# Kernel optimization log

Measured on AMD Instinct MI355X. Metric: run time of the kernel, lower is better.

The kernel has to match this reference:

```python
import jax, jax.numpy as jnp
import numpy as np

B, N, DIM = 1, 1024, 512
H, DH = 8, 64
TOPK_RATIO = 0.1
SCALE = DH ** -0.5
PH = 32  # phase MLP hidden = hidden_dim//2 = 64//2
INIT_SCALE = 0.02


def cayley(Mre, Mim):
    # CayleyLinear: unitary weight W = (I - A)^{-1} (I + A), A skew-Hermitian
    M = (Mre + 1j * Mim).astype(jnp.complex64) * INIT_SCALE
    A = M - M.conj().T
    I = jnp.eye(M.shape[0], dtype=M.dtype)
    return jnp.linalg.solve(I - A, I + A)


def phase_fn(mag, pw1, pb1, pw2, pb2):
    # PhaseModulation: MLP(|alpha|) + 0.1*|alpha| residual
    h = jax.nn.silu(mag[..., None] @ pw1 + pb1)  # (...,PH)
    out = (h @ pw2 + pb2)[..., 0]
    return out + mag * 0.1


def setup_inputs() -> dict:
    key = jax.random.key(0)
    ks = jax.random.split(key, 12)
    d = {
        'x_real': jax.random.normal(ks[0], (B, N, DIM), dtype=jnp.float32),
        'x_imag': jax.random.normal(ks[1], (B, N, DIM), dtype=jnp.float32),
    }
    for i, n in enumerate(['Wq', 'Wk', 'Wv', 'Wo']):
        d[n + '_re'] = jax.random.normal(ks[2 + 2 * i], (DIM, DIM), dtype=jnp.float32)
        d[n + '_im'] = jax.random.normal(ks[3 + 2 * i], (DIM, DIM), dtype=jnp.float32)
    d['pw1'] = jax.random.normal(ks[10], (1, PH), dtype=jnp.float32) * 0.1
    d['pb1'] = jnp.zeros((PH,), dtype=jnp.float32)
    d['pw2'] = jax.random.normal(ks[11], (PH, 1), dtype=jnp.float32) * 0.1
    d['pb2'] = jnp.zeros((1,), dtype=jnp.float32)
    return d


def reference(x_real, x_imag, Wq_re, Wq_im, Wk_re, Wk_im, Wv_re, Wv_im,
              Wo_re, Wo_im, pw1, pb1, pw2, pb2):
    x = (x_real + 1j * x_imag).astype(jnp.complex64)  # (B,N,D)
    Q = x @ cayley(Wq_re, Wq_im)
    K = x @ cayley(Wk_re, Wk_im)
    V = x @ cayley(Wv_re, Wv_im)
    # (B,N,D) -> (B,H,N,DH)
    Q = Q.reshape(B, N, H, DH).transpose(0, 2, 1, 3)
    K = K.reshape(B, N, H, DH).transpose(0, 2, 1, 3)
    V = V.reshape(B, N, H, DH).transpose(0, 2, 1, 3)
    # complex inner products: conj(Q) . K
    alpha = jnp.einsum('bhnd,bhsd->bhns', Q.conj(), K) * SCALE  # (B,H,N,N) complex
    mag = jnp.abs(alpha)
    phase = phase_fn(jax.lax.stop_gradient(mag), pw1, pb1, pw2, pb2)
    beta = alpha * jnp.exp(1j * phase.astype(jnp.complex64))
    # Born-rule normalization: p = |beta|^2 / sum |beta|^2
    b2 = beta.real ** 2 + beta.imag ** 2
    probs = b2 / b2.sum(axis=-1, keepdims=True)  # (B,H,N,N) real
    # top-k interference routing
    k = max(1, int(TOPK_RATIO * N))
    tp, ti = jax.lax.top_k(probs, k)  # (B,H,N,k)
    tpn = tp / (tp.sum(axis=-1, keepdims=True) + 1e-8)
    w = jax.nn.softmax(tpn * k, axis=-1)  # complex_softmax on real input
    # gather V rows per (b,h): (N,DH)[(N,k)] -> (N,k,DH), no NxN expand
    gather = jax.vmap(jax.vmap(lambda v, i: v[i]))
    V_topk = gather(V, ti)  # (B,H,N,k,DH) complex
    out = (w[..., None] * V_topk).sum(axis=3)  # (B,H,N,DH)
    out = out.transpose(0, 2, 1, 3).reshape(B, N, DIM)
    out = out @ cayley(Wo_re, Wo_im)
    return out  # complex64 (B,N,DIM)
```

## Files before the change

kernel.cpp:

```cpp
#include <hip/hip_runtime.h>
#include <math.h>


#define PLANE   262144
#define CMAT    524288
#define PPLANE  524288
#define CPROJ   1048576
#define KTOP    102

#define R_FLOATS 12582912
#define POOL_FLOATS (4*CMAT + 8192 + R_FLOATS)
__device__ __attribute__((aligned(256))) float g_pool[POOL_FLOATS];

__launch_bounds__(256)
__global__ void cgemm_kernel(
    const float* __restrict__ Are, const float* __restrict__ Aim, int sA,
    const float* __restrict__ Bre, const float* __restrict__ Bim, int sB,
    const float* __restrict__ Dre, const float* __restrict__ Dim, int sD,
    const float* __restrict__ Ere2, float* __restrict__ Ewr, int sE,
    float* __restrict__ Cre, float* __restrict__ Cim, int sC,
    int M, int N, int Kd, float dcoef, int mode, int out_floats)
{
    __shared__ float As_re[2][32][34], As_im[2][32][34];
    __shared__ float Bs_re[2][32][68], Bs_im[2][32][68];
    const int b = blockIdx.z;
    Are += (size_t)b * sA; Aim += (size_t)b * sA;
    Bre += (size_t)b * sB; Bim += (size_t)b * sB;
    Dre += (size_t)b * sD; Dim += (size_t)b * sD;
    const float* Ere = Ere2 + (size_t)b * sE;
    const float* Eim = Ere + PLANE;
    float* Uwr = Ewr ? (Ewr + (size_t)b * sE) : (float*)0;
    Cre += (size_t)b * sC; Cim += (size_t)b * sC;
    const int bnd = mode == 5 ? (out_floats - b * sC) : 0;
    const int tid = threadIdx.x;
    const int bm = blockIdx.y * 32, bn = blockIdx.x * 64;
    const int tm = (tid >> 4) << 1;
    const int tn = (tid & 15) << 2;
    const int lmA = tid >> 3;
    const int lkA = (tid & 7) << 2;
    const int lkB = tid >> 4;
    const int lnB = (tid & 15) << 2;
    float cr[2][4] = {{0.f}}, ci[2][4] = {{0.f}};
    const float* pAre = Are + (size_t)(bm + lmA) * Kd + lkA;
    const float* pAim = Aim + (size_t)(bm + lmA) * Kd + lkA;
    const float* pBre = Bre + (size_t)lkB * N + bn + lnB;
    const float* pBim = Bim + (size_t)lkB * N + bn + lnB;
    float4 ar  = *(const float4*)(pAre);
    float4 ai  = *(const float4*)(pAim);
    float4 br0 = *(const float4*)(pBre);
    float4 bi0 = *(const float4*)(pBim);
    float4 br1 = *(const float4*)(pBre + (size_t)16 * N);
    float4 bi1 = *(const float4*)(pBim + (size_t)16 * N);
    for (int k0 = 0; k0 < Kd; k0 += 32) {
        const int buf = (k0 >> 5) & 1;
        As_re[buf][lkA+0][lmA] = ar.x; As_re[buf][lkA+1][lmA] = ar.y;
        As_re[buf][lkA+2][lmA] = ar.z; As_re[buf][lkA+3][lmA] = ar.w;
        As_im[buf][lkA+0][lmA] = ai.x; As_im[buf][lkA+1][lmA] = ai.y;
        As_im[buf][lkA+2][lmA] = ai.z; As_im[buf][lkA+3][lmA] = ai.w;
        *(float4*)&Bs_re[buf][lkB][lnB] = br0;
        *(float4*)&Bs_im[buf][lkB][lnB] = bi0;
        *(float4*)&Bs_re[buf][lkB+16][lnB] = br1;
        *(float4*)&Bs_im[buf][lkB+16][lnB] = bi1;
        __syncthreads();
        const int kn = k0 + 32;
        if (kn < Kd) {
            ar  = *(const float4*)(pAre + kn);
            ai  = *(const float4*)(pAim + kn);
            br0 = *(const float4*)(pBre + (size_t)kn * N);
            bi0 = *(const float4*)(pBim + (size_t)kn * N);
            br1 = *(const float4*)(pBre + (size_t)(kn + 16) * N);
            bi1 = *(const float4*)(pBim + (size_t)(kn + 16) * N);
        }
        #pragma unroll
        for (int k = 0; k < 32; ++k) {
            const float2 xr = *(const float2*)&As_re[buf][k][tm];
            const float2 xi = *(const float2*)&As_im[buf][k][tm];
            const float4 yr = *(const float4*)&Bs_re[buf][k][tn];
            const float4 yi = *(const float4*)&Bs_im[buf][k][tn];
            const float axr[2] = {xr.x, xr.y};
            const float axi[2] = {xi.x, xi.y};
            const float byr[4] = {yr.x, yr.y, yr.z, yr.w};
            const float byi[4] = {yi.x, yi.y, yi.z, yi.w};
            #pragma unroll
            for (int i = 0; i < 2; ++i) {
                #pragma unroll
                for (int j = 0; j < 4; ++j) {
                    cr[i][j] += axr[i]*byr[j] - axi[i]*byi[j];
                    ci[i][j] += axr[i]*byi[j] + axi[i]*byr[j];
                }
            }
        }
    }
    #pragma unroll
    for (int i = 0; i < 2; ++i) {
        const int row = bm + tm + i;
        const size_t idx = (size_t)row * N + bn + tn;
        float vr[4] = {cr[i][0], cr[i][1], cr[i][2], cr[i][3]};
        float vi[4] = {ci[i][0], ci[i][1], ci[i][2], ci[i][3]};
        if (mode == 1) {
            const float4 dr4 = *(const float4*)(Dre + idx);
            const float4 di4 = *(const float4*)(Dim + idx);
            const float dr[4] = {dr4.x, dr4.y, dr4.z, dr4.w};
            const float di[4] = {di4.x, di4.y, di4.z, di4.w};
            #pragma unroll
            for (int j = 0; j < 4; ++j) { vr[j] = dcoef*dr[j] - vr[j]; vi[j] = dcoef*di[j] - vi[j]; }
        } else if (mode == 2) {
            const float4 dr4 = *(const float4*)(Dre + idx);
            const float4 di4 = *(const float4*)(Dim + idx);
            const float dr[4] = {dr4.x, dr4.y, dr4.z, dr4.w};
            const float di[4] = {di4.x, di4.y, di4.z, di4.w};
            float ur[4], ui[4];
            #pragma unroll
            for (int j = 0; j < 4; ++j) { ur[j] = 5.5f*dr[j] + 0.5f*vr[j]; ui[j] = 5.5f*di[j] + 0.5f*vi[j]; }
            *(float4*)(Uwr + idx) = make_float4(ur[0], ur[1], ur[2], ur[3]);
            *(float4*)(Uwr + PLANE + idx) = make_float4(ui[0], ui[1], ui[2], ui[3]);
        } else if (mode == 3) {
            const float inv61 = 1.0f/61.5f;
            const float4 sr4 = *(const float4*)(Dre + idx);
            const float4 si4 = *(const float4*)(Dim + idx);
            const float4 s2r = *(const float4*)(Ere + idx);
            const float4 s2i = *(const float4*)(Eim + idx);
            const float sr[4] = {sr4.x, sr4.y, sr4.z, sr4.w};
            const float si[4] = {si4.x, si4.y, si4.z, si4.w};
            const float tr[4] = {s2r.x, s2r.y, s2r.z, s2r.w};
            const float ti[4] = {s2i.x, s2i.y, s2i.z, s2i.w};
            #pragma unroll
            for (int j = 0; j < 4; ++j) {
                const float diag = (row == bn + tn + j) ? 60.5f : 0.0f;
                vr[j] = (diag + 48.f*sr[j] + 23.f*tr[j] + vr[j]) * inv61;
                vi[j] = (       48.f*si[j] + 23.f*ti[j] + vi[j]) * inv61;
            }
        } else if (mode == 4) {
            const float4 dr4 = *(const float4*)(Dre + idx);
            const float4 di4 = *(const float4*)(Dim + idx);
            const float dr[4] = {dr4.x, dr4.y, dr4.z, dr4.w};
            const float di[4] = {di4.x, di4.y, di4.z, di4.w};
            #pragma unroll
            for (int j = 0; j < 4; ++j) {
                const float diag = (row == bn + tn + j) ? 1.0f : 0.0f;
                vr[j] = 2.f*dr[j] + 2.f*vr[j] - diag;
                vi[j] = 2.f*di[j] + 2.f*vi[j];
            }
        }
        if (mode == 5) {
            #pragma unroll
            for (int j = 0; j < 4; ++j) {
                const size_t ire = idx + j;
                const size_t iim = (size_t)PPLANE + idx + j;
                if (ire < (size_t)bnd) Cre[ire] = vr[j];
                if (iim < (size_t)bnd) Cre[iim] = vi[j];
            }
        } else {
            *(float4*)(Cre + idx) = make_float4(vr[0], vr[1], vr[2], vr[3]);
            *(float4*)(Cim + idx) = make_float4(vi[0], vi[1], vi[2], vi[3]);
        }
    }
}

__launch_bounds__(256)
__global__ void build_A_kernel(const float* __restrict__ W0re, const float* __restrict__ W0im,
                               const float* __restrict__ W1re, const float* __restrict__ W1im,
                               const float* __restrict__ W2re, const float* __restrict__ W2im,
                               const float* __restrict__ W3re, const float* __restrict__ W3im,
                               int aoff)
{
    float* Aout = g_pool + aoff;
    const int w = blockIdx.y;
    const float* Mre; const float* Mim;
    if      (w == 0) { Mre = W0re; Mim = W0im; }
    else if (w == 1) { Mre = W1re; Mim = W1im; }
    else if (w == 2) { Mre = W2re; Mim = W2im; }
    else             { Mre = W3re; Mim = W3im; }
    const int idx = blockIdx.x * 256 + threadIdx.x;
    const int i = idx >> 9, j = idx & 511;
    float* Are = Aout + (size_t)w * CMAT;
    float* Aim = Are + PLANE;
    Are[idx] = 0.02f * (Mre[i*512 + j] - Mre[j*512 + i]);
    Aim[idx] = 0.02f * (Mim[i*512 + j] + Mim[j*512 + i]);
}

__launch_bounds__(256)
__global__ void zero_kernel(float* __restrict__ p, int n)
{
    const int i = blockIdx.x * 256 + threadIdx.x;
    if (i < n) p[i] = 0.f;
}

__launch_bounds__(256)
__global__ void scores_kernel(const float* __restrict__ Qre, const float* __restrict__ Qim,
                              const float* __restrict__ Kre, const float* __restrict__ Kim,
                              float* __restrict__ B2, float* __restrict__ RS)
{
    __shared__ float Qs_re[16][68], Qs_im[16][68], Ks_re[16][68], Ks_im[16][68];
    __shared__ float rs[64];
    const int h = blockIdx.z;
    const int bm = blockIdx.y * 64, bn = blockIdx.x * 64;
    const int tid = threadIdx.x;
    const int tm = (tid >> 4) << 2, tn = (tid & 15) << 2;
    const int lm = tid >> 2, lk = (tid & 3) << 2;
    float dr[4][4] = {{0.f}}, di[4][4] = {{0.f}};
    for (int k0 = 0; k0 < 64; k0 += 16) {
        const float4 qr = *(const float4*)(Qre + (size_t)(bm+lm)*512 + h*64 + k0 + lk);
        const float4 qi = *(const float4*)(Qim + (size_t)(bm+lm)*512 + h*64 + k0 + lk);
        const float4 kr = *(const float4*)(Kre + (size_t)(bn+lm)*512 + h*64 + k0 + lk);
        const float4 ki = *(const float4*)(Kim + (size_t)(bn+lm)*512 + h*64 + k0 + lk);
        __syncthreads();
        Qs_re[lk+0][lm]=qr.x; Qs_re[lk+1][lm]=qr.y; Qs_re[lk+2][lm]=qr.z; Qs_re[lk+3][lm]=qr.w;
        Qs_im[lk+0][lm]=qi.x; Qs_im[lk+1][lm]=qi.y; Qs_im[lk+2][lm]=qi.z; Qs_im[lk+3][lm]=qi.w;
        Ks_re[lk+0][lm]=kr.x; Ks_re[lk+1][lm]=kr.y; Ks_re[lk+2][lm]=kr.z; Ks_re[lk+3][lm]=kr.w;
        Ks_im[lk+0][lm]=ki.x; Ks_im[lk+1][lm]=ki.y; Ks_im[lk+2][lm]=ki.z; Ks_im[lk+3][lm]=ki.w;
        __syncthreads();
        #pragma unroll
        for (int k = 0; k < 16; ++k) {
            const float4 xr = *(const float4*)&Qs_re[k][tm];
            const float4 xi = *(const float4*)&Qs_im[k][tm];
            const float4 yr = *(const float4*)&Ks_re[k][tn];
            const float4 yi = *(const float4*)&Ks_im[k][tn];
            const float axr[4] = {xr.x, xr.y, xr.z, xr.w};
            const float axi[4] = {xi.x, xi.y, xi.z, xi.w};
            const float byr[4] = {yr.x, yr.y, yr.z, yr.w};
            const float byi[4] = {yi.x, yi.y, yi.z, yi.w};
            #pragma unroll
            for (int i = 0; i < 4; ++i) {
                #pragma unroll
                for (int j = 0; j < 4; ++j) {
                    dr[i][j] += axr[i]*byr[j] + axi[i]*byi[j];
                    di[i][j] += axr[i]*byi[j] - axi[i]*byr[j];
                }
            }
        }
    }
    if (tid < 64) rs[tid] = 0.f;
    __syncthreads();
    float rpart[4] = {0.f, 0.f, 0.f, 0.f};
    #pragma unroll
    for (int i = 0; i < 4; ++i) {
        #pragma unroll
        for (int j = 0; j < 4; ++j) {
            const float b2v = (dr[i][j]*dr[i][j] + di[i][j]*di[i][j]) * 0.015625f;
            B2[(size_t)h*1048576 + (size_t)(bm+tm+i)*1024 + (bn+tn+j)] = b2v;
            rpart[i] += b2v;
        }
    }
    #pragma unroll
    for (int i = 0; i < 4; ++i) atomicAdd(&rs[tm+i], rpart[i]);
    __syncthreads();
    if (tid < 64) atomicAdd(&RS[h*1024 + bm + tid], rs[tid]);
}

__launch_bounds__(256)
__global__ void select_kernel(const float* __restrict__ B2, const float* __restrict__ RS,
                              const float* __restrict__ Vre, const float* __restrict__ Vim,
                              float* __restrict__ AOre, float* __restrict__ AOim)
{
    __shared__ float sv[1024];
    __shared__ unsigned int hist[256];
    __shared__ int ssum[256];
    __shared__ unsigned int sc[4];
    __shared__ float sel_v[104];
    __shared__ int sel_i[104];
    __shared__ float sel_w[104];
    __shared__ float rbuf[256];
    const int bid = blockIdx.x;
    const int h = bid >> 10, n = bid & 1023;
    const int tid = threadIdx.x;
    const float* row = B2 + (size_t)h * 1048576 + (size_t)n * 1024;
    #pragma unroll
    for (int e = 0; e < 4; ++e) sv[tid + 256*e] = row[tid + 256*e];
    if (tid == 0) sc[2] = 0u;
    __syncthreads();

    unsigned prefix = 0u, pmask = 0u;
    int krem = KTOP;
    for (int pass = 0; pass < 4; ++pass) {
        const int shift = 24 - 8 * pass;
        hist[tid] = 0u;
        __syncthreads();
        #pragma unroll
        for (int e = 0; e < 4; ++e) {
            const unsigned u = __float_as_uint(sv[tid + 256*e]);
            if ((u & pmask) == prefix) atomicAdd(&hist[(u >> shift) & 255u], 1u);
        }
        __syncthreads();
        ssum[tid] = (int)hist[tid];
        __syncthreads();
        for (int off = 1; off < 256; off <<= 1) {
            const int add = (tid + off < 256) ? ssum[tid + off] : 0;
            __syncthreads();
            ssum[tid] += add;
            __syncthreads();
        }
        const int above = (tid < 255) ? ssum[tid + 1] : 0;
        if (ssum[tid] >= krem && above < krem) {
            sc[0] = (unsigned)tid;
            sc[1] = (unsigned)(krem - above);
        }
        __syncthreads();
        prefix |= sc[0] << shift;
        pmask |= 0xFFu << shift;
        krem = (int)sc[1];
        __syncthreads();
    }
    const unsigned T = prefix;
    const int m = krem;

    #pragma unroll
    for (int e = 0; e < 4; ++e) {
        const int i = tid + 256*e;
        const float v = sv[i];
        const unsigned u = __float_as_uint(v);
        bool sel = (u > T);
        if (!sel && u == T) {
            int rank = 0;
            for (int j = 0; j < i; ++j) rank += (__float_as_uint(sv[j]) == T) ? 1 : 0;
            sel = (rank < m);
        }
        if (sel) {
            const unsigned p = atomicAdd(&sc[2], 1u);
            if (p < 104u) { sel_v[p] = v; sel_i[p] = i; }
        }
    }
    __syncthreads();

    rbuf[tid] = (tid < KTOP) ? sel_v[tid] : 0.f;
    __syncthreads();
    for (int st = 128; st > 0; st >>= 1) { if (tid < st) rbuf[tid] += rbuf[tid + st]; __syncthreads(); }
    const float sumtop = rbuf[0];
    __syncthreads();
    rbuf[tid] = (tid < KTOP) ? sel_v[tid] : -1.f;
    __syncthreads();
    for (int st = 128; st > 0; st >>= 1) { if (tid < st) rbuf[tid] = fmaxf(rbuf[tid], rbuf[tid + st]); __syncthreads(); }
    const float vmax = rbuf[0];
    __syncthreads();

    const float S_row = RS[(h << 10) + n];
    const float denom = sumtop + 1e-8f * S_row;
    const float scl = (float)KTOP / denom;
    if (tid < KTOP) sel_w[tid] = expf(sel_v[tid] * scl - vmax * scl);
    __syncthreads();
    rbuf[tid] = (tid < KTOP) ? sel_w[tid] : 0.f;
    __syncthreads();
    for (int st = 128; st > 0; st >>= 1) { if (tid < st) rbuf[tid] += rbuf[tid + st]; __syncthreads(); }
    const float Z = rbuf[0];
    __syncthreads();

    if (tid < 128) {
        const int d = tid & 63;
        const int im = tid >> 6;
        const float* Vp = im ? Vim : Vre;
        const int base = h * 64 + d;
        float acc = 0.f;
        for (int j = 0; j < KTOP; ++j) acc += sel_w[j] * Vp[(size_t)sel_i[j] * 512 + base];
        acc /= Z;
        float* AOp = im ? AOim : AOre;
        AOp[(size_t)n * 512 + h * 64 + d] = acc;
    }
}

extern "C" void kernel_launch(void* const* d_in, const int* in_sizes, int n_in,
                              void* d_out, int out_size, void* d_ws, size_t ws_size,
                              hipStream_t stream)
{
    (void)in_sizes; (void)n_in; (void)d_ws; (void)ws_size;
    const float* x_re = (const float*)d_in[0];
    const float* x_im = (const float*)d_in[1];

    float* pool = nullptr;
    hipGetSymbolAddress((void**)&pool, HIP_SYMBOL(g_pool));

    float* Wall = pool;
    float* RSg  = Wall + 4*CMAT;
    float* R    = RSg + 8192;
    float* A  = R;
    float* S  = R + 4*CMAT;
    float* S2 = R + 8*CMAT;
    float* X  = R + 12*CMAT;
    float* X2 = R + 16*CMAT;
    float* T  = R + 20*CMAT;
    float* Q  = R;
    float* Kp = R + CPROJ;
    float* V  = R + 2*CPROJ;
    float* AO = R + 3*CPROJ;
    float* B2 = R + 4*CPROJ;

    const int aoff = (int)(A - pool);

    build_A_kernel<<<dim3(1024,4),256,0,stream>>>(
        (const float*)d_in[2],(const float*)d_in[3],(const float*)d_in[4],(const float*)d_in[5],
        (const float*)d_in[6],(const float*)d_in[7],(const float*)d_in[8],(const float*)d_in[9], aoff);
    cgemm_kernel<<<dim3(8,16,4),256,0,stream>>>(A,A+PLANE,CMAT, A,A+PLANE,CMAT,
                                                A,A+PLANE,CMAT, A,nullptr,CMAT,
                                                S,S+PLANE,CMAT, 512,512,512, 0.f, 0, 0);
    cgemm_kernel<<<dim3(8,16,4),256,0,stream>>>(S,S+PLANE,CMAT, S,S+PLANE,CMAT,
                                                S,S+PLANE,CMAT, S,X,CMAT,
                                                S2,S2+PLANE,CMAT, 512,512,512, 0.f, 2, 0);
    cgemm_kernel<<<dim3(8,16,4),256,0,stream>>>(S2,S2+PLANE,CMAT, X,X+PLANE,CMAT,
                                                S,S+PLANE,CMAT, S2,nullptr,CMAT,
                                                X2,X2+PLANE,CMAT, 512,512,512, 0.f, 3, 0);
    float* Xc = X2; float* Xn = X;
    for (int it = 0; it < 2; ++it) {
        cgemm_kernel<<<dim3(8,16,4),256,0,stream>>>(S,S+PLANE,CMAT, Xc,Xc+PLANE,CMAT,
                                                    Xc,Xc+PLANE,CMAT, S,nullptr,CMAT,
                                                    T,T+PLANE,CMAT, 512,512,512, 1.f, 1, 0);
        cgemm_kernel<<<dim3(8,16,4),256,0,stream>>>(Xc,Xc+PLANE,CMAT, T,T+PLANE,CMAT,
                                                    Xc,Xc+PLANE,CMAT, S,nullptr,CMAT,
                                                    Xn,Xn+PLANE,CMAT, 512,512,512, 2.f, 1, 0);
        float* tmp = Xc; Xc = Xn; Xn = tmp;
    }
    cgemm_kernel<<<dim3(8,16,4),256,0,stream>>>(A,A+PLANE,CMAT, Xc,Xc+PLANE,CMAT,
                                                Xc,Xc+PLANE,CMAT, S,nullptr,CMAT,
                                                Wall,Wall+PLANE,CMAT, 512,512,512, 0.f, 4, 0);

    cgemm_kernel<<<dim3(8,32,3),256,0,stream>>>(x_re,x_im,0, Wall,Wall+PLANE,CMAT,
                                                x_re,x_im,0, S,nullptr,0,
                                                Q,Q+PPLANE,CPROJ, 1024,512,512, 0.f, 0, 0);

    zero_kernel<<<32,256,0,stream>>>(RSg, 8192);
    scores_kernel<<<dim3(16,16,8),256,0,stream>>>(Q,Q+PPLANE, Kp,Kp+PPLANE, B2, RSg);
    select_kernel<<<8192,256,0,stream>>>(B2, RSg, V,V+PPLANE, AO,AO+PPLANE);

    cgemm_kernel<<<dim3(8,16,2),256,0,stream>>>(AO,AO+PPLANE,PLANE, Wall+3*CMAT,Wall+3*CMAT+PLANE,0,
                                                AO,AO+PPLANE,0, S,nullptr,0,
                                                (float*)d_out,nullptr,PLANE, 512,512,512, 0.f, 5, out_size);
}
```

Baseline: 1.003 ms.

## Use 64x64 register-tiled split-K complex GEMM for Cayley solve with combine pass

Replaces the 32x64-tile complex GEMM in the Cayley-inverse iteration chain with a new 64xTN tile kernel that computes 4x4 outputs per thread. Each K dimension is split in half, doubling the block count to keep the device filled, and a separate combine kernel sums the two partials and applies the per-mode epilogue. The Q/K/V projection also moves to the new kernel with 64x32 tiles. The split adds extra kernel launches and a round trip of partials through global memory in exchange for more arithmetic per load and better occupancy.

```diff
diff --git a/kernel.cpp b/kernel.cpp
--- a/kernel.cpp
+++ b/kernel.cpp
@@ -8,28 +8,185 @@
 #define CPROJ   1048576
 #define KTOP    102
 
-#define R_FLOATS 12582912
+#define R_FLOATS (28*CMAT)
 #define POOL_FLOATS (4*CMAT + 8192 + R_FLOATS)
 __device__ __attribute__((aligned(256))) float g_pool[POOL_FLOATS];
+
+template<int TN>
+__launch_bounds__(TN*4)
+__global__ void cgemm44_kernel(
+    const float* __restrict__ Are, const float* __restrict__ Aim, int sA,
+    const float* __restrict__ Bre, const float* __restrict__ Bim, int sB,
+    float* __restrict__ C0re, float* __restrict__ C0im,
+    float* __restrict__ P1re, float* __restrict__ P1im, int sC,
+    int N, int Kd, int split)
+{
+    __shared__ float As_re[2][32][66], As_im[2][32][66];
+    __shared__ float Bs_re[2][32][TN+4], Bs_im[2][32][TN+4];
+    const int z = blockIdx.z;
+    const int w  = split ? (z >> 1) : z;
+    const int kh = split ? (z & 1) : 0;
+    const int kbeg = kh * (Kd >> 1);
+    const int klen = split ? (Kd >> 1) : Kd;
+    Are += (size_t)w * sA; Aim += (size_t)w * sA;
+    Bre += (size_t)w * sB; Bim += (size_t)w * sB;
+    float* Cre = (kh ? P1re : C0re) + (size_t)w * sC;
+    float* Cim = (kh ? P1im : C0im) + (size_t)w * sC;
+    const int tid = threadIdx.x;
+    const int bm = blockIdx.y * 64, bn = blockIdx.x * TN;
+    const int tm = (tid / (TN/4)) << 2;
+    const int tn = (tid % (TN/4)) << 2;
+    constexpr int AQ = (TN == 64) ? 2 : 4;
+    const int lmA = (TN == 64) ? (tid >> 2) : (tid >> 1);
+    const int lkA = (TN == 64) ? ((tid & 3) << 3) : ((tid & 1) << 4);
+    const int lkB = (TN == 64) ? (tid >> 4) : (tid >> 3);
+    const int lnB = (TN == 64) ? ((tid & 15) << 2) : ((tid & 7) << 2);
+    float cr[4][4] = {{0.f}}, ci[4][4] = {{0.f}};
+    const float* pAre = Are + (size_t)(bm + lmA) * Kd + kbeg + lkA;
+    const float* pAim = Aim + (size_t)(bm + lmA) * Kd + kbeg + lkA;
+    const float* pBre = Bre + (size_t)(kbeg + lkB) * N + bn + lnB;
+    const float* pBim = Bim + (size_t)(kbeg + lkB) * N + bn + lnB;
+    float4 arv[AQ], aiv[AQ], brv0, biv0, brv1, biv1;
+    #pragma unroll
+    for (int q = 0; q < AQ; ++q) {
+        arv[q] = *(const float4*)(pAre + 4*q);
+        aiv[q] = *(const float4*)(pAim + 4*q);
+    }
+    brv0 = *(const float4*)(pBre);
+    biv0 = *(const float4*)(pBim);
+    brv1 = *(const float4*)(pBre + (size_t)16 * N);
+    biv1 = *(const float4*)(pBim + (size_t)16 * N);
+    for (int kk = 0; kk < klen; kk += 32) {
+        const int buf = (kk >> 5) & 1;
+        #pragma unroll
+        for (int q = 0; q < AQ; ++q) {
+            const int kb = lkA + 4*q;
+            As_re[buf][kb+0][lmA] = arv[q].x; As_re[buf][kb+1][lmA] = arv[q].y;
+            As_re[buf][kb+2][lmA] = arv[q].z; As_re[buf][kb+3][lmA] = arv[q].w;
+            As_im[buf][kb+0][lmA] = aiv[q].x; As_im[buf][kb+1][lmA] = aiv[q].y;
+            As_im[buf][kb+2][lmA] = aiv[q].z; As_im[buf][kb+3][lmA] = aiv[q].w;
+        }
+        *(float4*)&Bs_re[buf][lkB][lnB] = brv0;
+        *(float4*)&Bs_im[buf][lkB][lnB] = biv0;
+        *(float4*)&Bs_re[buf][lkB+16][lnB] = brv1;
+        *(float4*)&Bs_im[buf][lkB+16][lnB] = biv1;
+        __syncthreads();
+        const int knx = kk + 32;
+        if (knx < klen) {
+            #pragma unroll
+            for (int q = 0; q < AQ; ++q) {
+                arv[q] = *(const float4*)(pAre + knx + 4*q);
+                aiv[q] = *(const float4*)(pAim + knx + 4*q);
+            }
+            brv0 = *(const float4*)(pBre + (size_t)knx * N);
+            biv0 = *(const float4*)(pBim + (size_t)knx * N);
+            brv1 = *(const float4*)(pBre + (size_t)(knx + 16) * N);
+            biv1 = *(const float4*)(pBim + (size_t)(knx + 16) * N);
+        }
+        #pragma unroll
+        for (int k = 0; k < 32; ++k) {
+            const float4 xr = *(const float4*)&As_re[buf][k][tm];
+            const float4 xi = *(const float4*)&As_im[buf][k][tm];
+            const float4 yr = *(const float4*)&Bs_re[buf][k][tn];
+            const float4 yi = *(const float4*)&Bs_im[buf][k][tn];
+            const float axr[4] = {xr.x, xr.y, xr.z, xr.w};
+            const float axi[4] = {xi.x, xi.y, xi.z, xi.w};
+            const float byr[4] = {yr.x, yr.y, yr.z, yr.w};
+            const float byi[4] = {yi.x, yi.y, yi.z, yi.w};
+            #pragma unroll
+            for (int i = 0; i < 4; ++i) {
+                #pragma unroll
+                for (int j = 0; j < 4; ++j) {
+                    cr[i][j] += axr[i]*byr[j] - axi[i]*byi[j];
+                    ci[i][j] += axr[i]*byi[j] + axi[i]*byr[j];
+                }
+            }
+        }
+    }
+    #pragma unroll
+    for (int i = 0; i < 4; ++i) {
+        const size_t idx = (size_t)(bm + tm + i) * N + bn + tn;
+        *(float4*)(Cre + idx) = make_float4(cr[i][0], cr[i][1], cr[i][2], cr[i][3]);
+        *(float4*)(Cim + idx) = make_float4(ci[i][0], ci[i][1], ci[i][2], ci[i][3]);
+    }
+}
+
+__launch_bounds__(256)
+__global__ void combine_kernel(float* __restrict__ C, const float* __restrict__ P1,
+                               const float* __restrict__ D, const float* __restrict__ E,
+                               float* __restrict__ U, float dcoef, int mode)
+{
+    const size_t off = (size_t)blockIdx.y * CMAT;
+    const size_t idx = ((size_t)blockIdx.x * 256 + threadIdx.x) * 4;
+    const float4 p0r = *(const float4*)(C + off + idx);
+    const float4 p0i = *(const float4*)(C + off + PLANE + idx);
+    const float4 p1r = *(const float4*)(P1 + off + idx);
+    const float4 p1i = *(const float4*)(P1 + off + PLANE + idx);
+    float vr[4] = {p0r.x+p1r.x, p0r.y+p1r.y, p0r.z+p1r.z, p0r.w+p1r.w};
+    float vi[4] = {p0i.x+p1i.x, p0i.y+p1i.y, p0i.z+p1i.z, p0i.w+p1i.w};
+    const int row = (int)(idx >> 9);
+    const int col = (int)(idx & 511);
+    if (mode == 1) {
+        const float4 dr4 = *(const float4*)(D + off + idx);
+        const float4 di4 = *(const float4*)(D + off + PLANE + idx);
+        const float dr[4] = {dr4.x, dr4.y, dr4.z, dr4.w};
+        const float di[4] = {di4.x, di4.y, di4.z, di4.w};
+        #pragma unroll
+        for (int j = 0; j < 4; ++j) { vr[j] = dcoef*dr[j] - vr[j]; vi[j] = dcoef*di[j] - vi[j]; }
+    } else if (mode == 2) {
+        const float4 dr4 = *(const float4*)(D + off + idx);
+        const float4 di4 = *(const float4*)(D + off + PLANE + idx);
+        const float dr[4] = {dr4.x, dr4.y, dr4.z, dr4.w};
+        const float di[4] = {di4.x, di4.y, di4.z, di4.w};
+        float ur[4], ui[4];
+        #pragma unroll
+        for (int j = 0; j < 4; ++j) { ur[j] = 5.5f*dr[j] + 0.5f*vr[j]; ui[j] = 5.5f*di[j] + 0.5f*vi[j]; }
+        *(float4*)(U + off + idx) = make_float4(ur[0], ur[1], ur[2], ur[3]);
+        *(float4*)(U + off + PLANE + idx) = make_float4(ui[0], ui[1], ui[2], ui[3]);
+    } else if (mode == 3) {
+        const float inv61 = 1.0f/61.5f;
+        const float4 sr4 = *(const float4*)(D + off + idx);
+        const float4 si4 = *(const float4*)(D + off + PLANE + idx);
+        const float4 tr4 = *(const float4*)(E + off + idx);
+        const float4 ti4 = *(const float4*)(E + off + PLANE + idx);
+        const float sr[4] = {sr4.x, sr4.y, sr4.z, sr4.w};
+        const float si[4] = {si4.x, si4.y, si4.z, si4.w};
+        const float tr[4] = {tr4.x, tr4.y, tr4.z, tr4.w};
+        const float ti[4] = {ti4.x, ti4.y, ti4.z, ti4.w};
+        #pragma unroll
+        for (int j = 0; j < 4; ++j) {
+            const float diag = (row == col + j) ? 60.5f : 0.0f;
+            vr[j] = (diag + 48.f*sr[j] + 23.f*tr[j] + vr[j]) * inv61;
+            vi[j] = (       48.f*si[j] + 23.f*ti[j] + vi[j]) * inv61;
+        }
+    } else if (mode == 4) {
+        const float4 dr4 = *(const float4*)(D + off + idx);
+        const float4 di4 = *(const float4*)(D + off + PLANE + idx);
+        const float dr[4] = {dr4.x, dr4.y, dr4.z, dr4.w};
+        const float di[4] = {di4.x, di4.y, di4.z, di4.w};
+        #pragma unroll
+        for (int j = 0; j < 4; ++j) {
+            const float diag = (row == col + j) ? 1.0f : 0.0f;
+            vr[j] = 2.f*dr[j] + 2.f*vr[j] - diag;
+            vi[j] = 2.f*di[j] + 2.f*vi[j];
+        }
+    }
+    *(float4*)(C + off + idx) = make_float4(vr[0], vr[1], vr[2], vr[3]);
+    *(float4*)(C + off + PLANE + idx) = make_float4(vi[0], vi[1], vi[2], vi[3]);
+}
 
 __launch_bounds__(256)
 __global__ void cgemm_kernel(
     const float* __restrict__ Are, const float* __restrict__ Aim, int sA,
     const float* __restrict__ Bre, const float* __restrict__ Bim, int sB,
-    const float* __restrict__ Dre, const float* __restrict__ Dim, int sD,
-    const float* __restrict__ Ere2, float* __restrict__ Ewr, int sE,
     float* __restrict__ Cre, float* __restrict__ Cim, int sC,
-    int M, int N, int Kd, float dcoef, int mode, int out_floats)
+    int M, int N, int Kd, int mode, int out_floats)
 {
     __shared__ float As_re[2][32][34], As_im[2][32][34];
     __shared__ float Bs_re[2][32][68], Bs_im[2][32][68];
     const int b = blockIdx.z;
     Are += (size_t)b * sA; Aim += (size_t)b * sA;
     Bre += (size_t)b * sB; Bim += (size_t)b * sB;
-    Dre += (size_t)b * sD; Dim += (size_t)b * sD;
-    const float* Ere = Ere2 + (size_t)b * sE;
-    const float* Eim = Ere + PLANE;
-    float* Uwr = Ewr ? (Ewr + (size_t)b * sE) : (float*)0;
     Cre += (size_t)b * sC; Cim += (size_t)b * sC;
     const int bnd = mode == 5 ? (out_floats - b * sC) : 0;
     const int tid = threadIdx.x;
@@ -93,55 +250,9 @@
     }
     #pragma unroll
     for (int i = 0; i < 2; ++i) {
-        const int row = bm + tm + i;
-        const size_t idx = (size_t)row * N + bn + tn;
+        const size_t idx = (size_t)(bm + tm + i) * N + bn + tn;
         float vr[4] = {cr[i][0], cr[i][1], cr[i][2], cr[i][3]};
         float vi[4] = {ci[i][0], ci[i][1], ci[i][2], ci[i][3]};
-        if (mode == 1) {
-            const float4 dr4 = *(const float4*)(Dre + idx);
-            const float4 di4 = *(const float4*)(Dim + idx);
-            const float dr[4] = {dr4.x, dr4.y, dr4.z, dr4.w};
-            const float di[4] = {di4.x, di4.y, di4.z, di4.w};
-            #pragma unroll
-            for (int j = 0; j < 4; ++j) { vr[j] = dcoef*dr[j] - vr[j]; vi[j] = dcoef*di[j] - vi[j]; }
-        } else if (mode == 2) {
-            const float4 dr4 = *(const float4*)(Dre + idx);
-            const float4 di4 = *(const float4*)(Dim + idx);
-            const float dr[4] = {dr4.x, dr4.y, dr4.z, dr4.w};
-            const float di[4] = {di4.x, di4.y, di4.z, di4.w};
-            float ur[4], ui[4];
-            #pragma unroll
-            for (int j = 0; j < 4; ++j) { ur[j] = 5.5f*dr[j] + 0.5f*vr[j]; ui[j] = 5.5f*di[j] + 0.5f*vi[j]; }
-            *(float4*)(Uwr + idx) = make_float4(ur[0], ur[1], ur[2], ur[3]);
-            *(float4*)(Uwr + PLANE + idx) = make_float4(ui[0], ui[1], ui[2], ui[3]);
-        } else if (mode == 3) {
-            const float inv61 = 1.0f/61.5f;
-            const float4 sr4 = *(const float4*)(Dre + idx);
-            const float4 si4 = *(const float4*)(Dim + idx);
-            const float4 s2r = *(const float4*)(Ere + idx);
-            const float4 s2i = *(const float4*)(Eim + idx);
-            const float sr[4] = {sr4.x, sr4.y, sr4.z, sr4.w};
-            const float si[4] = {si4.x, si4.y, si4.z, si4.w};
-            const float tr[4] = {s2r.x, s2r.y, s2r.z, s2r.w};
-            const float ti[4] = {s2i.x, s2i.y, s2i.z, s2i.w};
-            #pragma unroll
-            for (int j = 0; j < 4; ++j) {
-                const float diag = (row == bn + tn + j) ? 60.5f : 0.0f;
-                vr[j] = (diag + 48.f*sr[j] + 23.f*tr[j] + vr[j]) * inv61;
-                vi[j] = (       48.f*si[j] + 23.f*ti[j] + vi[j]) * inv61;
-            }
-        } else if (mode == 4) {
-            const float4 dr4 = *(const float4*)(Dre + idx);
-            const float4 di4 = *(const float4*)(Dim + idx);
-            const float dr[4] = {dr4.x, dr4.y, dr4.z, dr4.w};
-            const float di[4] = {di4.x, di4.y, di4.z, di4.w};
-            #pragma unroll
-            for (int j = 0; j < 4; ++j) {
-                const float diag = (row == bn + tn + j) ? 1.0f : 0.0f;
-                vr[j] = 2.f*dr[j] + 2.f*vr[j] - diag;
-                vi[j] = 2.f*di[j] + 2.f*vi[j];
-            }
-        }
         if (mode == 5) {
             #pragma unroll
             for (int j = 0; j < 4; ++j) {
@@ -371,12 +482,13 @@
     float* Wall = pool;
     float* RSg  = Wall + 4*CMAT;
     float* R    = RSg + 8192;
-    float* A  = R;
-    float* S  = R + 4*CMAT;
-    float* S2 = R + 8*CMAT;
-    float* X  = R + 12*CMAT;
-    float* X2 = R + 16*CMAT;
-    float* T  = R + 20*CMAT;
+    float* A   = R;
+    float* S   = R + 4*CMAT;
+    float* S2  = R + 8*CMAT;
+    float* X   = R + 12*CMAT;
+    float* X2  = R + 16*CMAT;
+    float* T   = R + 20*CMAT;
+    float* P1g = R + 24*CMAT;
     float* Q  = R;
     float* Kp = R + CPROJ;
     float* V  = R + 2*CPROJ;
@@ -384,42 +496,44 @@
     float* B2 = R + 4*CPROJ;
 
     const int aoff = (int)(A - pool);
+    float* P1re = P1g; float* P1im = P1g + PLANE;
+    const dim3 gA(8, 8, 8);
+    const dim3 gC(256, 4);
 
     build_A_kernel<<<dim3(1024,4),256,0,stream>>>(
         (const float*)d_in[2],(const float*)d_in[3],(const float*)d_in[4],(const float*)d_in[5],
         (const float*)d_in[6],(const float*)d_in[7],(const float*)d_in[8],(const float*)d_in[9], aoff);
-    cgemm_kernel<<<dim3(8,16,4),256,0,stream>>>(A,A+PLANE,CMAT, A,A+PLANE,CMAT,
-                                                A,A+PLANE,CMAT, A,nullptr,CMAT,
-                                                S,S+PLANE,CMAT, 512,512,512, 0.f, 0, 0);
-    cgemm_kernel<<<dim3(8,16,4),256,0,stream>>>(S,S+PLANE,CMAT, S,S+PLANE,CMAT,
-                                                S,S+PLANE,CMAT, S,X,CMAT,
-                                                S2,S2+PLANE,CMAT, 512,512,512, 0.f, 2, 0);
-    cgemm_kernel<<<dim3(8,16,4),256,0,stream>>>(S2,S2+PLANE,CMAT, X,X+PLANE,CMAT,
-                                                S,S+PLANE,CMAT, S2,nullptr,CMAT,
-                                                X2,X2+PLANE,CMAT, 512,512,512, 0.f, 3, 0);
+    cgemm44_kernel<64><<<gA,256,0,stream>>>(A,A+PLANE,CMAT, A,A+PLANE,CMAT,
+                                            S,S+PLANE, P1re,P1im, CMAT, 512,512, 1);
+    combine_kernel<<<gC,256,0,stream>>>(S, P1g, nullptr, nullptr, nullptr, 0.f, 0);
+    cgemm44_kernel<64><<<gA,256,0,stream>>>(S,S+PLANE,CMAT, S,S+PLANE,CMAT,
+                                            S2,S2+PLANE, P1re,P1im, CMAT, 512,512, 1);
+    combine_kernel<<<gC,256,0,stream>>>(S2, P1g, S, nullptr, X, 0.f, 2);
+    cgemm44_kernel<64><<<gA,256,0,stream>>>(S2,S2+PLANE,CMAT, X,X+PLANE,CMAT,
+                                            X2,X2+PLANE, P1re,P1im, CMAT, 512,512, 1);
+    combine_kernel<<<gC,256,0,stream>>>(X2, P1g, S, S2, nullptr, 0.f, 3);
     float* Xc = X2; float* Xn = X;
     for (int it = 0; it < 2; ++it) {
-        cgemm_kernel<<<dim3(8,16,4),256,0,stream>>>(S,S+PLANE,CMAT, Xc,Xc+PLANE,CMAT,
-                                                    Xc,Xc+PLANE,CMAT, S,nullptr,CMAT,
-                                                    T,T+PLANE,CMAT, 512,512,512, 1.f, 1, 0);
-        cgemm_kernel<<<dim3(8,16,4),256,0,stream>>>(Xc,Xc+PLANE,CMAT, T,T+PLANE,CMAT,
-                                                    Xc,Xc+PLANE,CMAT, S,nullptr,CMAT,
-                                                    Xn,Xn+PLANE,CMAT, 512,512,512, 2.f, 1, 0);
+        cgemm44_kernel<64><<<gA,256,0,stream>>>(S,S+PLANE,CMAT, Xc,Xc+PLANE,CMAT,
+                                                T,T+PLANE, P1re,P1im, CMAT, 512,512, 1);
+        combine_kernel<<<gC,256,0,stream>>>(T, P1g, Xc, nullptr, nullptr, 1.f, 1);
+        cgemm44_kernel<64><<<gA,256,0,stream>>>(Xc,Xc+PLANE,CMAT, T,T+PLANE,CMAT,
+                                                Xn,Xn+PLANE, P1re,P1im, CMAT, 512,512, 1);
+        combine_kernel<<<gC,256,0,stream>>>(Xn, P1g, Xc, nullptr, nullptr, 2.f, 1);
         float* tmp = Xc; Xc = Xn; Xn = tmp;
     }
-    cgemm_kernel<<<dim3(8,16,4),256,0,stream>>>(A,A+PLANE,CMAT, Xc,Xc+PLANE,CMAT,
-                                                Xc,Xc+PLANE,CMAT, S,nullptr,CMAT,
-                                                Wall,Wall+PLANE,CMAT, 512,512,512, 0.f, 4, 0);
-
-    cgemm_kernel<<<dim3(8,32,3),256,0,stream>>>(x_re,x_im,0, Wall,Wall+PLANE,CMAT,
-                                                x_re,x_im,0, S,nullptr,0,
-                                                Q,Q+PPLANE,CPROJ, 1024,512,512, 0.f, 0, 0);
+    cgemm44_kernel<64><<<gA,256,0,stream>>>(A,A+PLANE,CMAT, Xc,Xc+PLANE,CMAT,
+                                            Wall,Wall+PLANE, P1re,P1im, CMAT, 512,512, 1);
+    combine_kernel<<<gC,256,0,stream>>>(Wall, P1g, Xc, nullptr, nullptr, 0.f, 4);
+
+    cgemm44_kernel<32><<<dim3(16,16,3),128,0,stream>>>(x_re,x_im,0, Wall,Wall+PLANE,CMAT,
+                                                       Q,Q+PPLANE, nullptr,nullptr, CPROJ,
+                                                       512,512, 0);
 
     zero_kernel<<<32,256,0,stream>>>(RSg, 8192);
     scores_kernel<<<dim3(16,16,8),256,0,stream>>>(Q,Q+PPLANE, Kp,Kp+PPLANE, B2, RSg);
     select_kernel<<<8192,256,0,stream>>>(B2, RSg, V,V+PPLANE, AO,AO+PPLANE);
 
     cgemm_kernel<<<dim3(8,16,2),256,0,stream>>>(AO,AO+PPLANE,PLANE, Wall+3*CMAT,Wall+3*CMAT+PLANE,0,
-                                                AO,AO+PPLANE,0, S,nullptr,0,
-                                                (float*)d_out,nullptr,PLANE, 512,512,512, 0.f, 5, out_size);
-}
+                                                (float*)d_out,nullptr,PLANE, 512,512,512, 5, out_size);
+}
```

New measurement: 1.199 ms. 1.2x slower.
